# Performance work log

Hardware: AMD Instinct MI355X
Metric: run time of the kernel (lower is better)

## Reference

```python
import jax, jax.numpy as jnp
import numpy as np

C, H1, H2, K, HOUT = 128, 4, 5, 3, 4  # h_dim, gat1 heads, gat2 heads, BAN k, BAN h_out
BN_EPS = 1e-5


def _gat(x, W, a_src, a_dst, bias, src, dst, mask, N):
    # PyG-style GATConv: x:[N,Fin], W:[Fin,H*C], a_*:[H,C], mask:[E] (1=valid edge)
    H, Ch = a_src.shape
    xh = (x @ W).reshape(N, H, Ch)
    es = jnp.einsum('nhc,hc->nh', xh, a_src)
    ed = jnp.einsum('nhc,hc->nh', xh, a_dst)
    e = jax.nn.leaky_relu(es[src] + ed[dst], 0.2)                      # [E,H]
    e = jnp.where(mask[:, None] > 0, e, -1e9)
    m = jax.ops.segment_max(e, dst, num_segments=N)                    # [N,H]
    p = jnp.exp(e - m[dst]) * mask[:, None]
    s = jax.ops.segment_sum(p, dst, num_segments=N)
    alpha = p / s[dst]                                                 # segment softmax over incoming edges
    out = jax.ops.segment_sum(xh[src] * alpha[:, :, None], dst, num_segments=N)
    return out.reshape(N, H * Ch) + bias


def _forward(cell_features, Wd, bd, W1, a1s, a1d, b1, Wl1, bl1, W2, a2s, a2d, b2, Wl2, bl2,
             Wfc, bfc, Whg, bhg, Wc, bc, Wv, bv, Wq, bq, h_mat, h_bias, bn_gamma, bn_beta,
             triplets, edge_index):
    N = triplets.shape[0]
    src0, dst0 = edge_index[0], edge_index[1]
    # clean_edge_index drops self loops; GATConv (PyG default) re-adds exactly one per node
    idx = jnp.arange(N, dtype=src0.dtype)
    src = jnp.concatenate([src0, idx])
    dst = jnp.concatenate([dst0, idx])
    mask = jnp.concatenate([(src0 != dst0).astype(jnp.float32), jnp.ones((N,), jnp.float32)])
    x = triplets[:, :4].astype(jnp.float32) @ Wd + bd                  # drug_linear
    h1 = jax.nn.elu(_gat(x, W1, a1s, a1d, b1, src, dst, mask, N)) @ Wl1 + bl1
    h2 = jax.nn.elu(_gat(h1, W2, a2s, a2d, b2, src, dst, mask, N)) @ Wl2 + bl2
    h = jnp.mean(h1 + h2, axis=0)                                      # [C] graph readout
    hg = jax.nn.relu(h @ Wfc + bfc) @ Whg + bhg                        # [C]
    c = jax.nn.relu(cell_features @ Wc + bc)                           # [B,C]
    B = c.shape[0]
    v = jnp.broadcast_to(hg, (B, C))
    # BANLayer (DrugBAN) with singleton v/q sequence length
    v_ = jax.nn.relu(v @ Wv + bv)                                      # [B,C*K]
    q_ = jax.nn.relu(c @ Wq + bq)
    att = jnp.einsum('hk,bk,bk->bh', h_mat, v_, q_) + h_bias           # [B,HOUT]
    fused = att.sum(axis=1, keepdims=True) * (v_ * q_)                 # sum over heads of bilinear pooling
    logits = fused.reshape(B, C, K).sum(axis=-1)                       # AvgPool1d(k)*k == group sum
    mu = logits.mean(axis=0)
    var = logits.var(axis=0)                                           # biased var, as torch BN
    return (logits - mu) / jnp.sqrt(var + BN_EPS) * bn_gamma + bn_beta


def setup_inputs():
    key = jax.random.key(0)
    ks = iter(jax.random.split(key, 40))
    N, E, B, CF = 20000, 500000, 256, 954
    def w(shape, fan):
        return jax.random.normal(next(ks), shape, jnp.float32) / np.sqrt(fan)
    return dict(
        cell_features=jax.random.normal(next(ks), (B, CF), jnp.float32),
        Wd=w((4, C), 4), bd=jnp.zeros((C,), jnp.float32),
        W1=w((C, H1 * C), C), a1s=w((H1, C), C), a1d=w((H1, C), C), b1=jnp.zeros((H1 * C,), jnp.float32),
        Wl1=w((H1 * C, C), H1 * C), bl1=jnp.zeros((C,), jnp.float32),
        W2=w((C, H2 * C), C), a2s=w((H2, C), C), a2d=w((H2, C), C), b2=jnp.zeros((H2 * C,), jnp.float32),
        Wl2=w((H2 * C, C), H2 * C), bl2=jnp.zeros((C,), jnp.float32),
        Wfc=w((C, 2 * C), C), bfc=jnp.zeros((2 * C,), jnp.float32),
        Whg=w((2 * C, C), 2 * C), bhg=jnp.zeros((C,), jnp.float32),
        Wc=w((CF, C), CF), bc=jnp.zeros((C,), jnp.float32),
        Wv=w((C, C * K), C), bv=jnp.zeros((C * K,), jnp.float32),
        Wq=w((C, C * K), C), bq=jnp.zeros((C * K,), jnp.float32),
        h_mat=w((HOUT, C * K), C * K), h_bias=jnp.zeros((HOUT,), jnp.float32),
        bn_gamma=jnp.ones((C,), jnp.float32), bn_beta=jnp.zeros((C,), jnp.float32),
        triplets=jax.random.randint(next(ks), (N, 4), 0, 10, dtype=jnp.int32),
        edge_index=jax.random.randint(next(ks), (2, E), 0, N, dtype=jnp.int32),
    )


def reference(cell_features, Wd, bd, W1, a1s, a1d, b1, Wl1, bl1, W2, a2s, a2d, b2, Wl2, bl2,
              Wfc, bfc, Whg, bhg, Wc, bc, Wv, bv, Wq, bq, h_mat, h_bias, bn_gamma, bn_beta,
              triplets, edge_index):
    return _forward(cell_features, Wd, bd, W1, a1s, a1d, b1, Wl1, bl1, W2, a2s, a2d, b2, Wl2, bl2,
                    Wfc, bfc, Whg, bhg, Wc, bc, Wv, bv, Wq, bq, h_mat, h_bias, bn_gamma, bn_beta,
                    triplets, edge_index)
```

## Files before the change

### kernel.cpp

```cpp
#include <hip/hip_runtime.h>
#include <hip/hip_bf16.h>
#include <math.h>

#define CDIV(a,b) (((a)+(b)-1)/(b))

typedef __attribute__((ext_vector_type(8))) short short8v;
typedef __attribute__((ext_vector_type(4))) float f32x4;

__device__ inline float bf2lo(unsigned u) { return __uint_as_float(u << 16); }
__device__ inline float bf2hi(unsigned u) { return __uint_as_float(u & 0xffff0000u); }

__global__ void k_prep(const float* __restrict__ W1, __hip_bfloat16* __restrict__ W1t,
                       const float* __restrict__ Wl1, __hip_bfloat16* __restrict__ Wl1t,
                       const float* __restrict__ W2, __hip_bfloat16* __restrict__ W2t,
                       const float* __restrict__ Wl2, __hip_bfloat16* __restrict__ Wl2t,
                       const float* __restrict__ Wc, float* __restrict__ Wct,
                       const float* __restrict__ Wq, float* __restrict__ Wqt) {
  int i = blockIdx.x * 256 + threadIdx.x;
  const int n1 = 128 * 512, n2 = 512 * 128, n3 = 128 * 640, n4 = 640 * 128;
  const int n5 = 954 * 128, n6 = 128 * 384;
  if (i < n1) { int m = i / 128, k = i % 128; W1t[i] = __float2bfloat16(W1[(size_t)k * 512 + m]); return; }
  i -= n1;
  if (i < n2) { int m = i / 512, k = i % 512; Wl1t[i] = __float2bfloat16(Wl1[(size_t)k * 128 + m]); return; }
  i -= n2;
  if (i < n3) { int m = i / 128, k = i % 128; W2t[i] = __float2bfloat16(W2[(size_t)k * 640 + m]); return; }
  i -= n3;
  if (i < n4) { int m = i / 640, k = i % 640; Wl2t[i] = __float2bfloat16(Wl2[(size_t)k * 128 + m]); return; }
  i -= n4;
  if (i < n5) { int m = i / 954, k = i % 954; Wct[i] = Wc[(size_t)k * 128 + m]; return; }
  i -= n5;
  if (i < n6) { int m = i / 128, k = i % 128; Wqt[i] = Wq[(size_t)k * 384 + m]; return; }
}

__global__ void k_drug(const int* __restrict__ trip, const float* __restrict__ Wd,
                       const float* __restrict__ bd, __hip_bfloat16* __restrict__ x, int N) {
  int i = blockIdx.x * 256 + threadIdx.x;
  if (i >= N * 128) return;
  int n = i >> 7, c = i & 127;
  const int* t = trip + n * 4;
  float acc = bd[c];
  acc += (float)t[0] * Wd[c] + (float)t[1] * Wd[128 + c] +
         (float)t[2] * Wd[256 + c] + (float)t[3] * Wd[384 + c];
  x[i] = __float2bfloat16(acc);
}

template <bool BIAS>
__global__ void k_gemm_mfma(const __hip_bfloat16* __restrict__ A,
                            const __hip_bfloat16* __restrict__ Bt,
                            const float* __restrict__ bias,
                            __hip_bfloat16* __restrict__ Cb,
                            int Nr, int K, int M) {
  __shared__ short As[64 * 40];
  __shared__ short Bs[64 * 40];
  int tid = threadIdx.x;
  int lane = tid & 63, wid = tid >> 6;
  int wr = wid >> 1, wc = wid & 1;
  int lrow = lane & 15, lkc = lane >> 4;
  int row0 = blockIdx.y * 64, col0 = blockIdx.x * 64;

  int arow = tid >> 2, akc = tid & 3;
  int grow = row0 + arow; if (grow >= Nr) grow = Nr - 1;
  const __hip_bfloat16* agp = A + (size_t)grow * K + akc * 8;
  const __hip_bfloat16* bgp = Bt + (size_t)(col0 + arow) * K + akc * 8;
  short* asp = &As[arow * 40 + akc * 8];
  short* bsp = &Bs[arow * 40 + akc * 8];

  f32x4 acc00 = {0.f,0.f,0.f,0.f}, acc01 = acc00, acc10 = acc00, acc11 = acc00;

  const short* a0p = &As[(wr * 32 + lrow) * 40 + lkc * 8];
  const short* a1p = &As[(wr * 32 + 16 + lrow) * 40 + lkc * 8];
  const short* b0p = &Bs[(wc * 32 + lrow) * 40 + lkc * 8];
  const short* b1p = &Bs[(wc * 32 + 16 + lrow) * 40 + lkc * 8];

  for (int k0 = 0; k0 < K; k0 += 32) {
    short8v av = *(const short8v*)(agp + k0);
    short8v bv = *(const short8v*)(bgp + k0);
    __syncthreads();
    *(short8v*)asp = av;
    *(short8v*)bsp = bv;
    __syncthreads();
    short8v a0 = *(const short8v*)a0p;
    short8v a1 = *(const short8v*)a1p;
    short8v b0 = *(const short8v*)b0p;
    short8v b1 = *(const short8v*)b1p;
    acc00 = __builtin_amdgcn_mfma_f32_16x16x32_bf16(a0, b0, acc00, 0, 0, 0);
    acc01 = __builtin_amdgcn_mfma_f32_16x16x32_bf16(a0, b1, acc01, 0, 0, 0);
    acc10 = __builtin_amdgcn_mfma_f32_16x16x32_bf16(a1, b0, acc10, 0, 0, 0);
    acc11 = __builtin_amdgcn_mfma_f32_16x16x32_bf16(a1, b1, acc11, 0, 0, 0);
  }

  int rbase = row0 + wr * 32 + (lane >> 4) * 4;
  int cbase = col0 + wc * 32 + lrow;
#pragma unroll
  for (int m = 0; m < 2; ++m) {
#pragma unroll
    for (int n = 0; n < 2; ++n) {
      f32x4 acc = m == 0 ? (n == 0 ? acc00 : acc01) : (n == 0 ? acc10 : acc11);
      int col = cbase + n * 16;
      int plane = col >> 7, ch = col & 127;
      float bv = BIAS ? bias[col] : 0.f;
      __hip_bfloat16* cp = Cb + (size_t)plane * Nr * 128 + ch;
#pragma unroll
      for (int r = 0; r < 4; ++r) {
        int grow2 = rbase + m * 16 + r;
        if (grow2 >= Nr) continue;
        cp[(size_t)grow2 * 128] = __float2bfloat16(acc[r] + bv);
      }
    }
  }
}

__global__ void k_dotmm(const float* __restrict__ A, const float* __restrict__ Bt,
                        const float* __restrict__ bias, float* __restrict__ C,
                        int Nr, int K, int M) {
  int wid = (blockIdx.x * blockDim.x + threadIdx.x) >> 6;
  int lane = threadIdx.x & 63;
  if (wid >= Nr * M) return;
  int b = wid / M, m = wid % M;
  const float* ar = A + (size_t)b * K;
  const float* br = Bt + (size_t)m * K;
  float acc = 0.f;
  for (int k = lane * 2; k + 1 < K; k += 128) {
    float2 av = *(const float2*)(ar + k);
    float2 bv = *(const float2*)(br + k);
    acc += av.x * bv.x + av.y * bv.y;
  }
#pragma unroll
  for (int off = 32; off; off >>= 1) acc += __shfl_xor(acc, off);
  if (lane == 0) C[wid] = fmaxf(acc + bias[m], 0.f);
}

__global__ void k_coef(const __hip_bfloat16* __restrict__ xh, const float* __restrict__ as_,
                       const float* __restrict__ ad_, float* __restrict__ es,
                       float* __restrict__ ed, int N, int H) {
  int wid = (blockIdx.x * blockDim.x + threadIdx.x) >> 6;
  int lane = threadIdx.x & 63;
  if (wid >= N * H) return;
  int h = wid / N, n = wid - h * N;
  const __hip_bfloat162* xp = (const __hip_bfloat162*)xh + (size_t)h * N * 64 + (size_t)n * 64;
  __hip_bfloat162 xv = xp[lane];
  float x0 = __bfloat162float(xv.x), x1 = __bfloat162float(xv.y);
  float2 a = ((const float2*)(as_ + h * 128))[lane];
  float2 d = ((const float2*)(ad_ + h * 128))[lane];
  float e1 = x0 * a.x + x1 * a.y;
  float e2 = x0 * d.x + x1 * d.y;
#pragma unroll
  for (int off = 32; off; off >>= 1) {
    e1 += __shfl_xor(e1, off);
    e2 += __shfl_xor(e2, off);
  }
  if (lane == 0) { es[(size_t)h * N + n] = e1; ed[(size_t)h * N + n] = e2; }
}

__global__ void k_deg(const int* __restrict__ src0, const int* __restrict__ dst0,
                      int* __restrict__ deg, int E) {
  int e = blockIdx.x * 256 + threadIdx.x;
  if (e >= E) return;
  int s = src0[e], d = dst0[e];
  if (s != d) atomicAdd(&deg[d], 1);
}

__global__ void k_scan(const int* __restrict__ deg, int* __restrict__ rowptr, int N) {
  __shared__ int part[1024];
  int t = threadIdx.x;
  int chunk = (N + 1023) >> 10;
  int b0 = t * chunk, b1 = min(N, b0 + chunk);
  int s = 0;
  for (int i = b0; i < b1; i++) s += deg[i];
  part[t] = s;
  __syncthreads();
  for (int off = 1; off < 1024; off <<= 1) {
    int v = (t >= off) ? part[t - off] : 0;
    __syncthreads();
    part[t] += v;
    __syncthreads();
  }
  int run = (t == 0) ? 0 : part[t - 1];
  for (int i = b0; i < b1; i++) { rowptr[i] = run; run += deg[i]; }
  if (b1 == N) rowptr[N] = run;
}

__global__ void k_fill_adj(const int* __restrict__ src0, const int* __restrict__ dst0,
                           const int* __restrict__ rowptr, int* __restrict__ cursor,
                           int* __restrict__ adj, int E) {
  int e = blockIdx.x * 256 + threadIdx.x;
  if (e >= E) return;
  int s = src0[e], d = dst0[e];
  if (s != d) {
    int pos = rowptr[d] + atomicAdd(&cursor[d], 1);
    adj[pos] = s;
  }
}

__global__ void k_gat_gather(const int* __restrict__ rowptr, const int* __restrict__ adj,
                             const float* __restrict__ es, const float* __restrict__ ed,
                             const __hip_bfloat16* __restrict__ xh,
                             const float* __restrict__ bias,
                             __hip_bfloat16* __restrict__ gout, int N, int H) {
  int wid = (blockIdx.x * blockDim.x + threadIdx.x) >> 6;
  int lane = threadIdx.x & 63;
  if (wid >= N * H) return;
  int h = wid / N, n = wid - h * N;
  int base = rowptr[n];
  int deg = rowptr[n + 1] - base;
  const float* esh = es + (size_t)h * N;
  float edn = ed[(size_t)h * N + n];
  float vself = esh[n] + edn;
  vself = vself > 0.f ? vself : 0.2f * vself;
  float m = vself;
  for (int i = lane; i < deg; i += 64) {
    int s = adj[base + i];
    float v = esh[s] + edn;
    v = v > 0.f ? v : 0.2f * v;
    m = fmaxf(m, v);
  }
#pragma unroll
  for (int off = 32; off; off >>= 1) m = fmaxf(m, __shfl_xor(m, off));
  const unsigned* xph = (const unsigned*)xh + (size_t)h * N * 64;
  float pself = __expf(vself - m);
  unsigned xs0 = xph[(size_t)n * 64 + lane];
  float a0 = pself * bf2lo(xs0);
  float a1 = pself * bf2hi(xs0);
  float b0 = 0.f, b1 = 0.f, c0 = 0.f, c1 = 0.f, d0 = 0.f, d1 = 0.f;
  float psum = (lane == 0) ? pself : 0.f;
  for (int c = 0; c < deg; c += 64) {
    int i = c + lane;
    int s = 0;
    float p = 0.f;
    if (i < deg) {
      s = adj[base + i];
      float v = esh[s] + edn;
      v = v > 0.f ? v : 0.2f * v;
      p = __expf(v - m);
      psum += p;
    }
    int cnt = min(64, deg - c);
    int j = 0;
    for (; j + 4 <= cnt; j += 4) {
      int s0 = __builtin_amdgcn_readlane(s, j);
      int s1 = __builtin_amdgcn_readlane(s, j + 1);
      int s2 = __builtin_amdgcn_readlane(s, j + 2);
      int s3 = __builtin_amdgcn_readlane(s, j + 3);
      float p0 = __int_as_float(__builtin_amdgcn_readlane(__float_as_int(p), j));
      float p1 = __int_as_float(__builtin_amdgcn_readlane(__float_as_int(p), j + 1));
      float p2 = __int_as_float(__builtin_amdgcn_readlane(__float_as_int(p), j + 2));
      float p3 = __int_as_float(__builtin_amdgcn_readlane(__float_as_int(p), j + 3));
      unsigned v0 = xph[(size_t)s0 * 64 + lane];
      unsigned v1 = xph[(size_t)s1 * 64 + lane];
      unsigned v2 = xph[(size_t)s2 * 64 + lane];
      unsigned v3 = xph[(size_t)s3 * 64 + lane];
      a0 += p0 * bf2lo(v0); a1 += p0 * bf2hi(v0);
      b0 += p1 * bf2lo(v1); b1 += p1 * bf2hi(v1);
      c0 += p2 * bf2lo(v2); c1 += p2 * bf2hi(v2);
      d0 += p3 * bf2lo(v3); d1 += p3 * bf2hi(v3);
    }
    for (; j < cnt; ++j) {
      int s0 = __builtin_amdgcn_readlane(s, j);
      float p0 = __int_as_float(__builtin_amdgcn_readlane(__float_as_int(p), j));
      unsigned v0 = xph[(size_t)s0 * 64 + lane];
      a0 += p0 * bf2lo(v0); a1 += p0 * bf2hi(v0);
    }
  }
  a0 += b0 + c0 + d0;
  a1 += b1 + c1 + d1;
#pragma unroll
  for (int off = 32; off; off >>= 1) psum += __shfl_xor(psum, off);
  float inv = 1.f / psum;
  float2 bv = ((const float2*)(bias + h * 128))[lane];
  float o0 = a0 * inv + bv.x;
  float o1 = a1 * inv + bv.y;
  o0 = o0 > 0.f ? o0 : expm1f(o0);
  o1 = o1 > 0.f ? o1 : expm1f(o1);
  __hip_bfloat162 r;
  r.x = __float2bfloat16(o0);
  r.y = __float2bfloat16(o1);
  ((__hip_bfloat162*)gout)[(size_t)n * (H * 64) + h * 64 + lane] = r;
}

__global__ void k_colsum(const __hip_bfloat16* __restrict__ A, float* __restrict__ colsum,
                         int N) {
  int c = threadIdx.x;
  int rows_per_block = CDIV(N, (int)gridDim.x);
  int r0 = blockIdx.x * rows_per_block;
  int r1 = min(N, r0 + rows_per_block);
  float acc = 0.f;
  for (int r = r0; r < r1; ++r) acc += __bfloat162float(A[(size_t)r * 128 + c]);
  atomicAdd(&colsum[c], acc);
}

__global__ void k_head(const float* __restrict__ colsum, const float* __restrict__ Wfc,
                       const float* __restrict__ bfc, const float* __restrict__ Whg,
                       const float* __restrict__ bhg, const float* __restrict__ Wv,
                       const float* __restrict__ bv, float* __restrict__ vvec, float invN) {
  __shared__ float h[128], t1[256], hg[128];
  int t = threadIdx.x;
  if (t < 128) h[t] = colsum[t] * invN;
  __syncthreads();
  float acc = bfc[t];
  for (int k = 0; k < 128; k++) acc += h[k] * Wfc[k * 256 + t];
  t1[t] = fmaxf(acc, 0.f);
  __syncthreads();
  if (t < 128) {
    float a2 = bhg[t];
    for (int k = 0; k < 256; k++) a2 += t1[k] * Whg[k * 128 + t];
    hg[t] = a2;
  }
  __syncthreads();
  for (int j = t; j < 384; j += 256) {
    float a3 = bv[j];
    for (int k = 0; k < 128; k++) a3 += hg[k] * Wv[k * 384 + j];
    vvec[j] = fmaxf(a3, 0.f);
  }
}

__global__ void k_fused(const float* __restrict__ vvec, const float* __restrict__ q,
                        const float* __restrict__ hmat, const float* __restrict__ hbias,
                        float* __restrict__ logits) {
  int b = blockIdx.x, c = threadIdx.x;
  __shared__ float red[128];
  float t[3];
  float part = 0.f;
#pragma unroll
  for (int j = 0; j < 3; j++) {
    int k = c * 3 + j;
    float hs = hmat[k] + hmat[384 + k] + hmat[768 + k] + hmat[1152 + k];
    t[j] = vvec[k] * q[(size_t)b * 384 + k];
    part += hs * t[j];
  }
  red[c] = part;
  __syncthreads();
  for (int s = 64; s > 0; s >>= 1) {
    if (c < s) red[c] += red[c + s];
    __syncthreads();
  }
  float attsum = red[0] + (hbias[0] + hbias[1] + hbias[2] + hbias[3]);
  logits[(size_t)b * 128 + c] = attsum * (t[0] + t[1] + t[2]);
}

__global__ void k_bn(const float* __restrict__ logits, const float* __restrict__ gamma,
                     const float* __restrict__ beta, float* __restrict__ out, int B) {
  int c = blockIdx.x, b = threadIdx.x;
  __shared__ float s1[256], s2[256];
  float v = logits[(size_t)b * 128 + c];
  s1[b] = v; s2[b] = v * v;
  __syncthreads();
  for (int s = B / 2; s > 0; s >>= 1) {
    if (b < s) { s1[b] += s1[b + s]; s2[b] += s2[b + s]; }
    __syncthreads();
  }
  float mu = s1[0] / B;
  float var = s2[0] / B - mu * mu;
  out[(size_t)b * 128 + c] = (v - mu) * rsqrtf(var + 1e-5f) * gamma[c] + beta[c];
}

extern "C" void kernel_launch(void* const* d_in, const int* in_sizes, int n_in,
                              void* d_out, int out_size, void* d_ws, size_t ws_size,
                              hipStream_t stream) {
  const float* cell = (const float*)d_in[0];
  const float* Wd   = (const float*)d_in[1];
  const float* bd   = (const float*)d_in[2];
  const float* W1   = (const float*)d_in[3];
  const float* a1s  = (const float*)d_in[4];
  const float* a1d  = (const float*)d_in[5];
  const float* b1   = (const float*)d_in[6];
  const float* Wl1  = (const float*)d_in[7];
  const float* bl1  = (const float*)d_in[8];
  const float* W2   = (const float*)d_in[9];
  const float* a2s  = (const float*)d_in[10];
  const float* a2d  = (const float*)d_in[11];
  const float* b2   = (const float*)d_in[12];
  const float* Wl2  = (const float*)d_in[13];
  const float* bl2  = (const float*)d_in[14];
  const float* Wfc  = (const float*)d_in[15];
  const float* bfc  = (const float*)d_in[16];
  const float* Whg  = (const float*)d_in[17];
  const float* bhg  = (const float*)d_in[18];
  const float* Wc   = (const float*)d_in[19];
  const float* bc   = (const float*)d_in[20];
  const float* Wv   = (const float*)d_in[21];
  const float* bv   = (const float*)d_in[22];
  const float* Wq   = (const float*)d_in[23];
  const float* bq   = (const float*)d_in[24];
  const float* hmat = (const float*)d_in[25];
  const float* hbias= (const float*)d_in[26];
  const float* gamma= (const float*)d_in[27];
  const float* beta = (const float*)d_in[28];
  const int* trip   = (const int*)d_in[29];
  const int* eidx   = (const int*)d_in[30];

  const int N = in_sizes[29] / 4;
  const int E = in_sizes[30] / 2;
  const int B = in_sizes[0] / 954;
  float* out = (float*)d_out;

  __hip_bfloat16* xb    = (__hip_bfloat16*)d_ws;
  __hip_bfloat16* xhb   = xb + (size_t)N * 128;
  __hip_bfloat16* goutb = xhb + (size_t)N * 640;
  __hip_bfloat16* h1b   = goutb + (size_t)N * 640;
  __hip_bfloat16* h2b   = h1b + (size_t)N * 128;
  __hip_bfloat16* W1t   = h2b + (size_t)N * 128;
  __hip_bfloat16* Wl1t  = W1t + 512 * 128;
  __hip_bfloat16* W2t   = Wl1t + 128 * 512;
  __hip_bfloat16* Wl2t  = W2t + 640 * 128;
  float* es     = (float*)(Wl2t + 128 * 640);
  float* ed     = es + (size_t)N * 5;
  float* colsum = ed + (size_t)N * 5;
  float* cbuf   = colsum + 128;
  float* qbuf   = cbuf + (size_t)B * 128;
  float* vvec   = qbuf + (size_t)B * 384;
  float* logits = vvec + 384;
  float* Wct    = logits + (size_t)B * 128;
  float* Wqt    = Wct + 128 * 954;
  int* rowptr   = (int*)(Wqt + 384 * 128);
  int* degb     = rowptr + (N + 1);
  int* cursor   = degb + N;
  int* adj      = cursor + N;

  const int* src0 = eidx;
  const int* dst0 = eidx + E;

  (void)hipMemsetAsync(colsum, 0, 128 * sizeof(float), stream);
  (void)hipMemsetAsync(degb, 0, (size_t)2 * N * sizeof(int), stream);

  {
    int tot = 128*512 + 512*128 + 128*640 + 640*128 + 954*128 + 128*384;
    k_prep<<<CDIV(tot, 256), 256, 0, stream>>>(W1, W1t, Wl1, Wl1t, W2, W2t, Wl2, Wl2t,
                                               Wc, Wct, Wq, Wqt);
  }

  k_deg<<<CDIV(E, 256), 256, 0, stream>>>(src0, dst0, degb, E);
  k_scan<<<1, 1024, 0, stream>>>(degb, rowptr, N);
  k_fill_adj<<<CDIV(E, 256), 256, 0, stream>>>(src0, dst0, rowptr, cursor, adj, E);

  k_drug<<<CDIV(N * 128, 256), 256, 0, stream>>>(trip, Wd, bd, xb, N);

  {
    dim3 g(512 / 64, CDIV(N, 64));
    k_gemm_mfma<false><<<g, 256, 0, stream>>>(xb, W1t, nullptr, xhb, N, 128, 512);
  }
  k_coef<<<CDIV(N * 4, 4), 256, 0, stream>>>(xhb, a1s, a1d, es, ed, N, 4);
  k_gat_gather<<<CDIV(N * 4, 4), 256, 0, stream>>>(rowptr, adj, es, ed, xhb, b1, goutb, N, 4);
  {
    dim3 g(128 / 64, CDIV(N, 64));
    k_gemm_mfma<true><<<g, 256, 0, stream>>>(goutb, Wl1t, bl1, h1b, N, 512, 128);
  }
  k_colsum<<<256, 128, 0, stream>>>(h1b, colsum, N);

  {
    dim3 g(640 / 64, CDIV(N, 64));
    k_gemm_mfma<false><<<g, 256, 0, stream>>>(h1b, W2t, nullptr, xhb, N, 128, 640);
  }
  k_coef<<<CDIV(N * 5, 4), 256, 0, stream>>>(xhb, a2s, a2d, es, ed, N, 5);
  k_gat_gather<<<CDIV(N * 5, 4), 256, 0, stream>>>(rowptr, adj, es, ed, xhb, b2, goutb, N, 5);
  {
    dim3 g(128 / 64, CDIV(N, 64));
    k_gemm_mfma<true><<<g, 256, 0, stream>>>(goutb, Wl2t, bl2, h2b, N, 640, 128);
  }
  k_colsum<<<256, 128, 0, stream>>>(h2b, colsum, N);

  k_head<<<1, 256, 0, stream>>>(colsum, Wfc, bfc, Whg, bhg, Wv, bv, vvec, 1.0f / N);
  k_dotmm<<<CDIV(B * 128, 4), 256, 0, stream>>>(cell, Wct, bc, cbuf, B, 954, 128);
  k_dotmm<<<CDIV(B * 384, 4), 256, 0, stream>>>(cbuf, Wqt, bq, qbuf, B, 128, 384);
  k_fused<<<B, 128, 0, stream>>>(vvec, qbuf, hmat, hbias, logits);
  k_bn<<<128, B, 0, stream>>>(logits, gamma, beta, out, B);
}
```

Baseline: 564.5 us.

## Split wavefront into half-waves gathering two neighbours with 8-byte loads

Restructures the GAT neighbour gather so each half of the wavefront handles a different neighbour row with 8-byte vector loads, then combines the halves with a cross-half shuffle. Adds a single-pass fast path for nodes with degree at most 64 that fuses the max and exp passes and avoids re-reading the adjacency. Also remaps block indices in an XCD-aware swizzle so consecutive waves land on the same chiplet for cache locality. In exchange it adds shuffle reductions, duplicated ELU work in the idle half, and a hard-coded four-waves-per-block assumption in the index mapping.

```diff
diff --git a/kernel.cpp b/kernel.cpp
--- a/kernel.cpp
+++ b/kernel.cpp
@@ -6,9 +6,14 @@
 
 typedef __attribute__((ext_vector_type(8))) short short8v;
 typedef __attribute__((ext_vector_type(4))) float f32x4;
+typedef __attribute__((ext_vector_type(2))) unsigned int uint2v;
 
 __device__ inline float bf2lo(unsigned u) { return __uint_as_float(u << 16); }
 __device__ inline float bf2hi(unsigned u) { return __uint_as_float(u & 0xffff0000u); }
+__device__ inline float leaky(float v) { return v > 0.f ? v : 0.2f * v; }
+__device__ inline float rlanef(float p, int j) {
+  return __int_as_float(__builtin_amdgcn_readlane(__float_as_int(p), j));
+}
 
 __global__ void k_prep(const float* __restrict__ W1, __hip_bfloat16* __restrict__ W1t,
                        const float* __restrict__ Wl1, __hip_bfloat16* __restrict__ Wl1t,
@@ -192,12 +197,50 @@
   }
 }
 
+__device__ __forceinline__ void pair_accum(const char* xbase, int loff, int half,
+                                           int s, float p, int cnt,
+                                           float& a0, float& a1, float& a2, float& a3,
+                                           float& b0, float& b1, float& b2, float& b3) {
+  int j = 0;
+  for (; j + 4 <= cnt; j += 4) {
+    int sL0 = __builtin_amdgcn_readlane(s, j);
+    int sH0 = __builtin_amdgcn_readlane(s, j + 1);
+    int sL1 = __builtin_amdgcn_readlane(s, j + 2);
+    int sH1 = __builtin_amdgcn_readlane(s, j + 3);
+    float pL0 = rlanef(p, j), pH0 = rlanef(p, j + 1);
+    float pL1 = rlanef(p, j + 2), pH1 = rlanef(p, j + 3);
+    int r0 = half ? sH0 : sL0;
+    int r1 = half ? sH1 : sL1;
+    float q0 = half ? pH0 : pL0;
+    float q1 = half ? pH1 : pL1;
+    uint2v u0 = *(const uint2v*)(xbase + (size_t)r0 * 256 + loff);
+    uint2v u1 = *(const uint2v*)(xbase + (size_t)r1 * 256 + loff);
+    a0 += q0 * bf2lo(u0.x); a1 += q0 * bf2hi(u0.x);
+    a2 += q0 * bf2lo(u0.y); a3 += q0 * bf2hi(u0.y);
+    b0 += q1 * bf2lo(u1.x); b1 += q1 * bf2hi(u1.x);
+    b2 += q1 * bf2lo(u1.y); b3 += q1 * bf2hi(u1.y);
+  }
+  for (; j < cnt; j += 2) {
+    int sL = __builtin_amdgcn_readlane(s, j);
+    int sH = __builtin_amdgcn_readlane(s, j + 1);
+    float pL = rlanef(p, j);
+    float pH = rlanef(p, j + 1);
+    int r0 = half ? sH : sL;
+    float q0 = half ? pH : pL;
+    uint2v u0 = *(const uint2v*)(xbase + (size_t)r0 * 256 + loff);
+    a0 += q0 * bf2lo(u0.x); a1 += q0 * bf2hi(u0.x);
+    a2 += q0 * bf2lo(u0.y); a3 += q0 * bf2hi(u0.y);
+  }
+}
+
 __global__ void k_gat_gather(const int* __restrict__ rowptr, const int* __restrict__ adj,
                              const float* __restrict__ es, const float* __restrict__ ed,
                              const __hip_bfloat16* __restrict__ xh,
                              const float* __restrict__ bias,
                              __hip_bfloat16* __restrict__ gout, int N, int H) {
-  int wid = (blockIdx.x * blockDim.x + threadIdx.x) >> 6;
+  int nb = gridDim.x, bx = blockIdx.x;
+  int sb = ((nb & 7) == 0) ? ((bx & 7) * (nb >> 3) + (bx >> 3)) : bx;
+  int wid = sb * 4 + (threadIdx.x >> 6);
   int lane = threadIdx.x & 63;
   if (wid >= N * H) return;
   int h = wid / N, n = wid - h * N;
@@ -205,76 +248,78 @@
   int deg = rowptr[n + 1] - base;
   const float* esh = es + (size_t)h * N;
   float edn = ed[(size_t)h * N + n];
-  float vself = esh[n] + edn;
-  vself = vself > 0.f ? vself : 0.2f * vself;
-  float m = vself;
-  for (int i = lane; i < deg; i += 64) {
-    int s = adj[base + i];
-    float v = esh[s] + edn;
-    v = v > 0.f ? v : 0.2f * v;
-    m = fmaxf(m, v);
-  }
-#pragma unroll
-  for (int off = 32; off; off >>= 1) m = fmaxf(m, __shfl_xor(m, off));
-  const unsigned* xph = (const unsigned*)xh + (size_t)h * N * 64;
-  float pself = __expf(vself - m);
-  unsigned xs0 = xph[(size_t)n * 64 + lane];
-  float a0 = pself * bf2lo(xs0);
-  float a1 = pself * bf2hi(xs0);
-  float b0 = 0.f, b1 = 0.f, c0 = 0.f, c1 = 0.f, d0 = 0.f, d1 = 0.f;
-  float psum = (lane == 0) ? pself : 0.f;
-  for (int c = 0; c < deg; c += 64) {
-    int i = c + lane;
-    int s = 0;
-    float p = 0.f;
-    if (i < deg) {
-      s = adj[base + i];
-      float v = esh[s] + edn;
-      v = v > 0.f ? v : 0.2f * v;
-      p = __expf(v - m);
-      psum += p;
+  float vself = leaky(esh[n] + edn);
+  const char* xbase = (const char*)xh + (size_t)h * N * 256;
+  int half = lane >> 5, l5 = lane & 31, loff = l5 * 8;
+
+  float a0 = 0.f, a1 = 0.f, a2 = 0.f, a3 = 0.f;
+  float b0 = 0.f, b1 = 0.f, b2 = 0.f, b3 = 0.f;
+  float psum, pself, m;
+
+  if (deg <= 64) {
+    int s = 0; float v = -1e30f;
+    if (lane < deg) { s = adj[base + lane]; v = leaky(esh[s] + edn); }
+    m = fmaxf(vself, v);
+#pragma unroll
+    for (int off = 32; off; off >>= 1) m = fmaxf(m, __shfl_xor(m, off));
+    float p = (lane < deg) ? __expf(v - m) : 0.f;
+    pself = __expf(vself - m);
+    psum = p;
+    pair_accum(xbase, loff, half, s, p, deg, a0, a1, a2, a3, b0, b1, b2, b3);
+  } else {
+    m = vself;
+    for (int i = lane; i < deg; i += 64) {
+      int s = adj[base + i];
+      m = fmaxf(m, leaky(esh[s] + edn));
     }
-    int cnt = min(64, deg - c);
-    int j = 0;
-    for (; j + 4 <= cnt; j += 4) {
-      int s0 = __builtin_amdgcn_readlane(s, j);
-      int s1 = __builtin_amdgcn_readlane(s, j + 1);
-      int s2 = __builtin_amdgcn_readlane(s, j + 2);
-      int s3 = __builtin_amdgcn_readlane(s, j + 3);
-      float p0 = __int_as_float(__builtin_amdgcn_readlane(__float_as_int(p), j));
-      float p1 = __int_as_float(__builtin_amdgcn_readlane(__float_as_int(p), j + 1));
-      float p2 = __int_as_float(__builtin_amdgcn_readlane(__float_as_int(p), j + 2));
-      float p3 = __int_as_float(__builtin_amdgcn_readlane(__float_as_int(p), j + 3));
-      unsigned v0 = xph[(size_t)s0 * 64 + lane];
-      unsigned v1 = xph[(size_t)s1 * 64 + lane];
-      unsigned v2 = xph[(size_t)s2 * 64 + lane];
-      unsigned v3 = xph[(size_t)s3 * 64 + lane];
-      a0 += p0 * bf2lo(v0); a1 += p0 * bf2hi(v0);
-      b0 += p1 * bf2lo(v1); b1 += p1 * bf2hi(v1);
-      c0 += p2 * bf2lo(v2); c1 += p2 * bf2hi(v2);
-      d0 += p3 * bf2lo(v3); d1 += p3 * bf2hi(v3);
+#pragma unroll
+    for (int off = 32; off; off >>= 1) m = fmaxf(m, __shfl_xor(m, off));
+    pself = __expf(vself - m);
+    psum = 0.f;
+    for (int c = 0; c < deg; c += 64) {
+      int i = c + lane;
+      int s = 0; float p = 0.f;
+      if (i < deg) {
+        s = adj[base + i];
+        p = __expf(leaky(esh[s] + edn) - m);
+        psum += p;
+      }
+      pair_accum(xbase, loff, half, s, p, min(64, deg - c), a0, a1, a2, a3, b0, b1, b2, b3);
     }
-    for (; j < cnt; ++j) {
-      int s0 = __builtin_amdgcn_readlane(s, j);
-      float p0 = __int_as_float(__builtin_amdgcn_readlane(__float_as_int(p), j));
-      unsigned v0 = xph[(size_t)s0 * 64 + lane];
-      a0 += p0 * bf2lo(v0); a1 += p0 * bf2hi(v0);
-    }
-  }
-  a0 += b0 + c0 + d0;
-  a1 += b1 + c1 + d1;
+  }
+
+  {
+    uint2v u = *(const uint2v*)(xbase + (size_t)n * 256 + loff);
+    float q = half ? 0.f : pself;
+    a0 += q * bf2lo(u.x); a1 += q * bf2hi(u.x);
+    a2 += q * bf2lo(u.y); a3 += q * bf2hi(u.y);
+  }
 #pragma unroll
   for (int off = 32; off; off >>= 1) psum += __shfl_xor(psum, off);
+  psum += pself;
+  a0 += b0; a1 += b1; a2 += b2; a3 += b3;
+  a0 += __shfl_xor(a0, 32);
+  a1 += __shfl_xor(a1, 32);
+  a2 += __shfl_xor(a2, 32);
+  a3 += __shfl_xor(a3, 32);
   float inv = 1.f / psum;
-  float2 bv = ((const float2*)(bias + h * 128))[lane];
+  float4 bv = ((const float4*)(bias + h * 128))[l5];
   float o0 = a0 * inv + bv.x;
   float o1 = a1 * inv + bv.y;
+  float o2 = a2 * inv + bv.z;
+  float o3 = a3 * inv + bv.w;
   o0 = o0 > 0.f ? o0 : expm1f(o0);
   o1 = o1 > 0.f ? o1 : expm1f(o1);
-  __hip_bfloat162 r;
-  r.x = __float2bfloat16(o0);
-  r.y = __float2bfloat16(o1);
-  ((__hip_bfloat162*)gout)[(size_t)n * (H * 64) + h * 64 + lane] = r;
+  o2 = o2 > 0.f ? o2 : expm1f(o2);
+  o3 = o3 > 0.f ? o3 : expm1f(o3);
+  if (half == 0) {
+    __hip_bfloat162 r01, r23;
+    r01.x = __float2bfloat16(o0); r01.y = __float2bfloat16(o1);
+    r23.x = __float2bfloat16(o2); r23.y = __float2bfloat16(o3);
+    __hip_bfloat162* gp = (__hip_bfloat162*)(gout + (size_t)n * (H * 128) + h * 128 + l5 * 4);
+    gp[0] = r01;
+    gp[1] = r23;
+  }
 }
 
 __global__ void k_colsum(const __hip_bfloat16* __restrict__ A, float* __restrict__ colsum,
```

After: 554.3 us. Within noise of the previous version (-1.8%).

## Fuse column-sum into GEMM epilogue, fold memsets into prep, restructure GAT gather

Applied to the files above, without the earlier changes.

The column-sum readout moves into the epilogue of the output-projection GEMM: per-wave shuffle reductions followed by atomics replace the two separate k_colsum passes. The two hipMemsetAsync calls are folded into the weight-prep kernel. The GAT gather gains a single-pass fast path for nodes with degree at most 64, an 8-way unrolled neighbour accumulation that reads padded lanes with zero weight, and a block-index swizzle intended to group nearby nodes on the same XCD. The aim is fewer launches, less re-reading of outputs and more memory-level parallelism in the gather, at the cost of extra atomics and wasted loads for padded neighbours.

```diff
diff --git a/kernel.cpp b/kernel.cpp
--- a/kernel.cpp
+++ b/kernel.cpp
@@ -9,13 +9,18 @@
 
 __device__ inline float bf2lo(unsigned u) { return __uint_as_float(u << 16); }
 __device__ inline float bf2hi(unsigned u) { return __uint_as_float(u & 0xffff0000u); }
+__device__ inline float leaky(float v) { return v > 0.f ? v : 0.2f * v; }
+__device__ inline float rlanef(float p, int j) {
+  return __int_as_float(__builtin_amdgcn_readlane(__float_as_int(p), j));
+}
 
 __global__ void k_prep(const float* __restrict__ W1, __hip_bfloat16* __restrict__ W1t,
                        const float* __restrict__ Wl1, __hip_bfloat16* __restrict__ Wl1t,
                        const float* __restrict__ W2, __hip_bfloat16* __restrict__ W2t,
                        const float* __restrict__ Wl2, __hip_bfloat16* __restrict__ Wl2t,
                        const float* __restrict__ Wc, float* __restrict__ Wct,
-                       const float* __restrict__ Wq, float* __restrict__ Wqt) {
+                       const float* __restrict__ Wq, float* __restrict__ Wqt,
+                       float* __restrict__ colsum, int* __restrict__ degz, int N) {
   int i = blockIdx.x * 256 + threadIdx.x;
   const int n1 = 128 * 512, n2 = 512 * 128, n3 = 128 * 640, n4 = 640 * 128;
   const int n5 = 954 * 128, n6 = 128 * 384;
@@ -30,6 +35,10 @@
   if (i < n5) { int m = i / 954, k = i % 954; Wct[i] = Wc[(size_t)k * 128 + m]; return; }
   i -= n5;
   if (i < n6) { int m = i / 128, k = i % 128; Wqt[i] = Wq[(size_t)k * 384 + m]; return; }
+  i -= n6;
+  if (i < 128) { colsum[i] = 0.f; return; }
+  i -= 128;
+  if (i < 2 * N) { degz[i] = 0; return; }
 }
 
 __global__ void k_drug(const int* __restrict__ trip, const float* __restrict__ Wd,
@@ -44,18 +53,19 @@
   x[i] = __float2bfloat16(acc);
 }
 
-template <bool BIAS>
+template <bool BIAS, bool COLSUM>
 __global__ void k_gemm_mfma(const __hip_bfloat16* __restrict__ A,
                             const __hip_bfloat16* __restrict__ Bt,
                             const float* __restrict__ bias,
                             __hip_bfloat16* __restrict__ Cb,
+                            float* __restrict__ colsum,
                             int Nr, int K, int M) {
   __shared__ short As[64 * 40];
   __shared__ short Bs[64 * 40];
   int tid = threadIdx.x;
   int lane = tid & 63, wid = tid >> 6;
   int wr = wid >> 1, wc = wid & 1;
-  int lrow = lane & 15, lkc = lane >> 4;
+  int lrow = lane & 15;
   int row0 = blockIdx.y * 64, col0 = blockIdx.x * 64;
 
   int arow = tid >> 2, akc = tid & 3;
@@ -67,6 +77,7 @@
 
   f32x4 acc00 = {0.f,0.f,0.f,0.f}, acc01 = acc00, acc10 = acc00, acc11 = acc00;
 
+  int lkc = lane >> 4;
   const short* a0p = &As[(wr * 32 + lrow) * 40 + lkc * 8];
   const short* a1p = &As[(wr * 32 + 16 + lrow) * 40 + lkc * 8];
   const short* b0p = &Bs[(wc * 32 + lrow) * 40 + lkc * 8];
@@ -91,6 +102,7 @@
 
   int rbase = row0 + wr * 32 + (lane >> 4) * 4;
   int cbase = col0 + wc * 32 + lrow;
+  float part0 = 0.f, part1 = 0.f;
 #pragma unroll
   for (int m = 0; m < 2; ++m) {
 #pragma unroll
@@ -104,8 +116,18 @@
       for (int r = 0; r < 4; ++r) {
         int grow2 = rbase + m * 16 + r;
         if (grow2 >= Nr) continue;
-        cp[(size_t)grow2 * 128] = __float2bfloat16(acc[r] + bv);
+        float v = acc[r] + bv;
+        cp[(size_t)grow2 * 128] = __float2bfloat16(v);
+        if (COLSUM) { if (n == 0) part0 += v; else part1 += v; }
       }
+    }
+  }
+  if (COLSUM) {
+    part0 += __shfl_xor(part0, 16); part0 += __shfl_xor(part0, 32);
+    part1 += __shfl_xor(part1, 16); part1 += __shfl_xor(part1, 32);
+    if (lane < 16) {
+      atomicAdd(&colsum[cbase], part0);
+      atomicAdd(&colsum[cbase + 16], part1);
     }
   }
 }
@@ -192,12 +214,46 @@
   }
 }
 
+__device__ __forceinline__ void acc8(const char* xbase, int loff, int s, float p, int j,
+                                     float& a0, float& a1) {
+  int s0 = __builtin_amdgcn_readlane(s, j);
+  int s1 = __builtin_amdgcn_readlane(s, j + 1);
+  int s2 = __builtin_amdgcn_readlane(s, j + 2);
+  int s3 = __builtin_amdgcn_readlane(s, j + 3);
+  int s4 = __builtin_amdgcn_readlane(s, j + 4);
+  int s5 = __builtin_amdgcn_readlane(s, j + 5);
+  int s6 = __builtin_amdgcn_readlane(s, j + 6);
+  int s7 = __builtin_amdgcn_readlane(s, j + 7);
+  unsigned u0 = *(const unsigned*)(xbase + (size_t)s0 * 256 + loff);
+  unsigned u1 = *(const unsigned*)(xbase + (size_t)s1 * 256 + loff);
+  unsigned u2 = *(const unsigned*)(xbase + (size_t)s2 * 256 + loff);
+  unsigned u3 = *(const unsigned*)(xbase + (size_t)s3 * 256 + loff);
+  unsigned u4 = *(const unsigned*)(xbase + (size_t)s4 * 256 + loff);
+  unsigned u5 = *(const unsigned*)(xbase + (size_t)s5 * 256 + loff);
+  unsigned u6 = *(const unsigned*)(xbase + (size_t)s6 * 256 + loff);
+  unsigned u7 = *(const unsigned*)(xbase + (size_t)s7 * 256 + loff);
+  float p0 = rlanef(p, j),     p1 = rlanef(p, j + 1);
+  float p2 = rlanef(p, j + 2), p3 = rlanef(p, j + 3);
+  float p4 = rlanef(p, j + 4), p5 = rlanef(p, j + 5);
+  float p6 = rlanef(p, j + 6), p7 = rlanef(p, j + 7);
+  a0 += p0 * bf2lo(u0); a1 += p0 * bf2hi(u0);
+  a0 += p1 * bf2lo(u1); a1 += p1 * bf2hi(u1);
+  a0 += p2 * bf2lo(u2); a1 += p2 * bf2hi(u2);
+  a0 += p3 * bf2lo(u3); a1 += p3 * bf2hi(u3);
+  a0 += p4 * bf2lo(u4); a1 += p4 * bf2hi(u4);
+  a0 += p5 * bf2lo(u5); a1 += p5 * bf2hi(u5);
+  a0 += p6 * bf2lo(u6); a1 += p6 * bf2hi(u6);
+  a0 += p7 * bf2lo(u7); a1 += p7 * bf2hi(u7);
+}
+
 __global__ void k_gat_gather(const int* __restrict__ rowptr, const int* __restrict__ adj,
                              const float* __restrict__ es, const float* __restrict__ ed,
                              const __hip_bfloat16* __restrict__ xh,
                              const float* __restrict__ bias,
                              __hip_bfloat16* __restrict__ gout, int N, int H) {
-  int wid = (blockIdx.x * blockDim.x + threadIdx.x) >> 6;
+  int nb = gridDim.x, bx = blockIdx.x;
+  int sb = ((nb & 7) == 0) ? ((bx & 7) * (nb >> 3) + (bx >> 3)) : bx;
+  int wid = sb * 4 + (threadIdx.x >> 6);
   int lane = threadIdx.x & 63;
   if (wid >= N * H) return;
   int h = wid / N, n = wid - h * N;
@@ -205,66 +261,53 @@
   int deg = rowptr[n + 1] - base;
   const float* esh = es + (size_t)h * N;
   float edn = ed[(size_t)h * N + n];
-  float vself = esh[n] + edn;
-  vself = vself > 0.f ? vself : 0.2f * vself;
-  float m = vself;
-  for (int i = lane; i < deg; i += 64) {
-    int s = adj[base + i];
-    float v = esh[s] + edn;
-    v = v > 0.f ? v : 0.2f * v;
-    m = fmaxf(m, v);
-  }
-#pragma unroll
-  for (int off = 32; off; off >>= 1) m = fmaxf(m, __shfl_xor(m, off));
-  const unsigned* xph = (const unsigned*)xh + (size_t)h * N * 64;
-  float pself = __expf(vself - m);
-  unsigned xs0 = xph[(size_t)n * 64 + lane];
-  float a0 = pself * bf2lo(xs0);
-  float a1 = pself * bf2hi(xs0);
-  float b0 = 0.f, b1 = 0.f, c0 = 0.f, c1 = 0.f, d0 = 0.f, d1 = 0.f;
-  float psum = (lane == 0) ? pself : 0.f;
-  for (int c = 0; c < deg; c += 64) {
-    int i = c + lane;
-    int s = 0;
-    float p = 0.f;
-    if (i < deg) {
-      s = adj[base + i];
-      float v = esh[s] + edn;
-      v = v > 0.f ? v : 0.2f * v;
-      p = __expf(v - m);
-      psum += p;
+  float vself = leaky(esh[n] + edn);
+  const char* xbase = (const char*)xh + (size_t)h * N * 256;
+  int loff = lane * 4;
+
+  float a0 = 0.f, a1 = 0.f;
+  float psum = 0.f, pself, m;
+
+  if (deg <= 64) {
+    int s = 0; float v = -3e38f;
+    if (lane < deg) { s = adj[base + lane]; v = leaky(esh[s] + edn); }
+    m = fmaxf(vself, v);
+#pragma unroll
+    for (int off = 32; off; off >>= 1) m = fmaxf(m, __shfl_xor(m, off));
+    float p = (lane < deg) ? __expf(v - m) : 0.f;
+    pself = __expf(vself - m);
+    psum = p;
+    for (int j = 0; j < deg; j += 8) acc8(xbase, loff, s, p, j, a0, a1);
+  } else {
+    m = vself;
+    for (int i = lane; i < deg; i += 64) {
+      int s = adj[base + i];
+      m = fmaxf(m, leaky(esh[s] + edn));
     }
-    int cnt = min(64, deg - c);
-    int j = 0;
-    for (; j + 4 <= cnt; j += 4) {
-      int s0 = __builtin_amdgcn_readlane(s, j);
-      int s1 = __builtin_amdgcn_readlane(s, j + 1);
-      int s2 = __builtin_amdgcn_readlane(s, j + 2);
-      int s3 = __builtin_amdgcn_readlane(s, j + 3);
-      float p0 = __int_as_float(__builtin_amdgcn_readlane(__float_as_int(p), j));
-      float p1 = __int_as_float(__builtin_amdgcn_readlane(__float_as_int(p), j + 1));
-      float p2 = __int_as_float(__builtin_amdgcn_readlane(__float_as_int(p), j + 2));
-      float p3 = __int_as_float(__builtin_amdgcn_readlane(__float_as_int(p), j + 3));
-      unsigned v0 = xph[(size_t)s0 * 64 + lane];
-      unsigned v1 = xph[(size_t)s1 * 64 + lane];
-      unsigned v2 = xph[(size_t)s2 * 64 + lane];
-      unsigned v3 = xph[(size_t)s3 * 64 + lane];
-      a0 += p0 * bf2lo(v0); a1 += p0 * bf2hi(v0);
-      b0 += p1 * bf2lo(v1); b1 += p1 * bf2hi(v1);
-      c0 += p2 * bf2lo(v2); c1 += p2 * bf2hi(v2);
-      d0 += p3 * bf2lo(v3); d1 += p3 * bf2hi(v3);
+#pragma unroll
+    for (int off = 32; off; off >>= 1) m = fmaxf(m, __shfl_xor(m, off));
+    pself = __expf(vself - m);
+    for (int c = 0; c < deg; c += 64) {
+      int i = c + lane;
+      int s = 0; float p = 0.f;
+      if (i < deg) {
+        s = adj[base + i];
+        p = __expf(leaky(esh[s] + edn) - m);
+        psum += p;
+      }
+      int cnt = min(64, deg - c);
+      for (int j = 0; j < cnt; j += 8) acc8(xbase, loff, s, p, j, a0, a1);
     }
-    for (; j < cnt; ++j) {
-      int s0 = __builtin_amdgcn_readlane(s, j);
-      float p0 = __int_as_float(__builtin_amdgcn_readlane(__float_as_int(p), j));
-      unsigned v0 = xph[(size_t)s0 * 64 + lane];
-      a0 += p0 * bf2lo(v0); a1 += p0 * bf2hi(v0);
-    }
-  }
-  a0 += b0 + c0 + d0;
-  a1 += b1 + c1 + d1;
+  }
+
+  {
+    unsigned u = *(const unsigned*)(xbase + (size_t)n * 256 + loff);
+    a0 += pself * bf2lo(u);
+    a1 += pself * bf2hi(u);
+  }
 #pragma unroll
   for (int off = 32; off; off >>= 1) psum += __shfl_xor(psum, off);
+  psum += pself;
   float inv = 1.f / psum;
   float2 bv = ((const float2*)(bias + h * 128))[lane];
   float o0 = a0 * inv + bv.x;
@@ -274,18 +317,7 @@
   __hip_bfloat162 r;
   r.x = __float2bfloat16(o0);
   r.y = __float2bfloat16(o1);
-  ((__hip_bfloat162*)gout)[(size_t)n * (H * 64) + h * 64 + lane] = r;
-}
-
-__global__ void k_colsum(const __hip_bfloat16* __restrict__ A, float* __restrict__ colsum,
-                         int N) {
-  int c = threadIdx.x;
-  int rows_per_block = CDIV(N, (int)gridDim.x);
-  int r0 = blockIdx.x * rows_per_block;
-  int r1 = min(N, r0 + rows_per_block);
-  float acc = 0.f;
-  for (int r = r0; r < r1; ++r) acc += __bfloat162float(A[(size_t)r * 128 + c]);
-  atomicAdd(&colsum[c], acc);
+  ((__hip_bfloat162*)(gout + (size_t)n * (H * 128) + h * 128))[lane] = r;
 }
 
 __global__ void k_head(const float* __restrict__ colsum, const float* __restrict__ Wfc,
@@ -419,13 +451,10 @@
   const int* src0 = eidx;
   const int* dst0 = eidx + E;
 
-  (void)hipMemsetAsync(colsum, 0, 128 * sizeof(float), stream);
-  (void)hipMemsetAsync(degb, 0, (size_t)2 * N * sizeof(int), stream);
-
-  {
-    int tot = 128*512 + 512*128 + 128*640 + 640*128 + 954*128 + 128*384;
+  {
+    int tot = 128*512 + 512*128 + 128*640 + 640*128 + 954*128 + 128*384 + 128 + 2 * N;
     k_prep<<<CDIV(tot, 256), 256, 0, stream>>>(W1, W1t, Wl1, Wl1t, W2, W2t, Wl2, Wl2t,
-                                               Wc, Wct, Wq, Wqt);
+                                               Wc, Wct, Wq, Wqt, colsum, degb, N);
   }
 
   k_deg<<<CDIV(E, 256), 256, 0, stream>>>(src0, dst0, degb, E);
@@ -436,27 +465,25 @@
 
   {
     dim3 g(512 / 64, CDIV(N, 64));
-    k_gemm_mfma<false><<<g, 256, 0, stream>>>(xb, W1t, nullptr, xhb, N, 128, 512);
+    k_gemm_mfma<false, false><<<g, 256, 0, stream>>>(xb, W1t, nullptr, xhb, nullptr, N, 128, 512);
   }
   k_coef<<<CDIV(N * 4, 4), 256, 0, stream>>>(xhb, a1s, a1d, es, ed, N, 4);
   k_gat_gather<<<CDIV(N * 4, 4), 256, 0, stream>>>(rowptr, adj, es, ed, xhb, b1, goutb, N, 4);
   {
     dim3 g(128 / 64, CDIV(N, 64));
-    k_gemm_mfma<true><<<g, 256, 0, stream>>>(goutb, Wl1t, bl1, h1b, N, 512, 128);
-  }
-  k_colsum<<<256, 128, 0, stream>>>(h1b, colsum, N);
+    k_gemm_mfma<true, true><<<g, 256, 0, stream>>>(goutb, Wl1t, bl1, h1b, colsum, N, 512, 128);
+  }
 
   {
     dim3 g(640 / 64, CDIV(N, 64));
-    k_gemm_mfma<false><<<g, 256, 0, stream>>>(h1b, W2t, nullptr, xhb, N, 128, 640);
+    k_gemm_mfma<false, false><<<g, 256, 0, stream>>>(h1b, W2t, nullptr, xhb, nullptr, N, 128, 640);
   }
   k_coef<<<CDIV(N * 5, 4), 256, 0, stream>>>(xhb, a2s, a2d, es, ed, N, 5);
   k_gat_gather<<<CDIV(N * 5, 4), 256, 0, stream>>>(rowptr, adj, es, ed, xhb, b2, goutb, N, 5);
   {
     dim3 g(128 / 64, CDIV(N, 64));
-    k_gemm_mfma<true><<<g, 256, 0, stream>>>(goutb, Wl2t, bl2, h2b, N, 640, 128);
-  }
-  k_colsum<<<256, 128, 0, stream>>>(h2b, colsum, N);
+    k_gemm_mfma<true, true><<<g, 256, 0, stream>>>(goutb, Wl2t, bl2, h2b, colsum, N, 640, 128);
+  }
 
   k_head<<<1, 256, 0, stream>>>(colsum, Wfc, bfc, Whg, bhg, Wv, bv, vvec, 1.0f / N);
   k_dotmm<<<CDIV(B * 128, 4), 256, 0, stream>>>(cell, Wct, bc, cbuf, B, 954, 128);
```

After: 499.4 us. 11.5% less time.
